# Optimization experiments

Measured on AMD Instinct MI355X. Metric: run time of the kernel, lower is better.

## Reference

```python
import jax, jax.numpy as jnp
import numpy as np

B, T, C = 2, 2048, 1024
NH = 16
HS = C // NH


def setup_inputs() -> dict:
    key = jax.random.key(0)
    k1, k2, k3 = jax.random.split(key, 3)
    scale = 1.0 / np.sqrt(C)
    return {
        "x": jax.random.normal(k1, (B, T, C), dtype=jnp.float32),
        "W_attn": jax.random.normal(k2, (C, 3 * C), dtype=jnp.float32) * scale,
        "b_attn": jnp.zeros((3 * C,), dtype=jnp.float32),
        "W_proj": jax.random.normal(k3, (C, C), dtype=jnp.float32) * scale,
        "b_proj": jnp.zeros((C,), dtype=jnp.float32),
    }


def reference(x, W_attn, b_attn, W_proj, b_proj) -> jnp.ndarray:
    Bx, Tx, Cx = x.shape
    qkv = x @ W_attn + b_attn                      # [B, T, 3C]
    q, k, v = jnp.split(qkv, 3, axis=-1)           # each [B, T, C]

    def heads(t):  # [B, T, C] -> [B, NH, T, HS]
        return t.reshape(Bx, Tx, NH, HS).transpose(0, 2, 1, 3)

    q, k, v = heads(q), heads(k), heads(v)
    att = jnp.einsum("bhqd,bhkd->bhqk", q, k) / jnp.sqrt(jnp.float32(HS))
    causal = jnp.tril(jnp.ones((Tx, Tx), dtype=bool))
    att = jnp.where(causal, att, -jnp.inf)
    att = jax.nn.softmax(att, axis=-1)
    y = jnp.einsum("bhqk,bhkd->bhqd", att, v)      # [B, NH, T, HS]
    y = y.transpose(0, 2, 1, 3).reshape(Bx, Tx, Cx)
    return y @ W_proj + b_proj
```

## Files before the change

kernel.cpp:

```cpp
#include <hip/hip_runtime.h>
#include <hip/hip_bf16.h>
#include <stdint.h>

#define DEV static __device__ __forceinline__

typedef __attribute__((ext_vector_type(8))) __bf16 bf16x8;
typedef __attribute__((ext_vector_type(4))) __bf16 bf16x4;
typedef __attribute__((ext_vector_type(4))) float f32x4;
typedef __attribute__((ext_vector_type(16))) float f32x16;

#define BB 2
#define TT 2048
#define CC 1024
#define NHH 16
#define HSS 64
#define BT 4096
#define N3 3072

DEV unsigned short f2bf(float f) {
  union { float f; uint32_t u; } v; v.f = f;
  uint32_t r = v.u + 0x7FFFu + ((v.u >> 16) & 1u);
  return (unsigned short)(r >> 16);
}

typedef const __attribute__((address_space(1))) unsigned int* gas_t;
typedef __attribute__((address_space(3))) unsigned int* las_t;

DEV void glds16(const void* g, void* l) {
  __builtin_amdgcn_global_load_lds((gas_t)g, (las_t)l, 16, 0, 0);
}

DEV f32x4 mfma16(bf16x8 a, bf16x8 b, f32x4 c) {
  return __builtin_amdgcn_mfma_f32_16x16x32_bf16(a, b, c, 0, 0, 0);
}
DEV f32x16 mfma32(bf16x8 a, bf16x8 b, f32x16 c) {
  return __builtin_amdgcn_mfma_f32_32x32x16_bf16(a, b, c, 0, 0, 0);
}

DEV bf16x8 ld8(const unsigned short* p) { return *(const bf16x8*)p; }

DEV f32x16 z16() {
  f32x16 v;
#pragma unroll
  for (int i = 0; i < 16; i++) v[i] = 0.f;
  return v;
}

__global__ __launch_bounds__(256) void k_prep(const float* __restrict__ x,
                                              const float* __restrict__ Wa,
                                              const float* __restrict__ Wp,
                                              unsigned short* __restrict__ xb,
                                              unsigned short* __restrict__ wabt,
                                              unsigned short* __restrict__ wpbt) {
  const int bid = blockIdx.x;
  const int t = threadIdx.x;
  if (bid < 1024) {
    int i = bid * 256 + t;
    const int n4 = BT * CC / 4;
#pragma unroll
    for (int r = 0; r < 4; r++, i += 262144) {
      if (i < n4) {
        float4 v = ((const float4*)x)[i];
        ushort4 o;
        o.x = f2bf(v.x); o.y = f2bf(v.y); o.z = f2bf(v.z); o.w = f2bf(v.w);
        ((ushort4*)xb)[i] = o;
      }
    }
    return;
  }
  __shared__ float tile[32][33];
  const float* in;
  unsigned short* out;
  int N, tid;
  if (bid < 4096) { in = Wa; out = wabt; N = N3; tid = bid - 1024; }
  else            { in = Wp; out = wpbt; N = CC; tid = bid - 4096; }
  const int ntx = N / 32;
  const int n0 = (tid % ntx) * 32, k0 = (tid / ntx) * 32;
  const int tx = t & 31, ty = t >> 5;
  for (int r = ty; r < 32; r += 8)
    tile[r][tx] = in[(size_t)(k0 + r) * N + n0 + tx];
  __syncthreads();
  for (int r = ty; r < 32; r += 8)
    out[(size_t)(n0 + r) * CC + k0 + tx] = f2bf(tile[tx][r]);
}

template <int OUT_BF16>
__global__ __launch_bounds__(512) void k_gemm(const unsigned short* __restrict__ A,
                                              const unsigned short* __restrict__ Bt,
                                              const float* __restrict__ bias,
                                              void* __restrict__ Cout,
                                              unsigned short* __restrict__ vtOut,
                                              int N, int K, int Rm, int Rn, int Xn) {
  __shared__ __align__(16) unsigned short As[3][128 * 32];
  __shared__ __align__(16) unsigned short Bs[3][128 * 32];
  const int t = threadIdx.x;
  const int wave = t >> 6, l = t & 63, lr = l & 15, lg = l >> 4;
  const int xcd = (int)blockIdx.x & 7, q = (int)blockIdx.x >> 3;
  const int m0 = ((xcd / Xn) * Rm + (q % Rm)) * 128;
  const int n0 = ((xcd % Xn) * Rn + (q / Rm)) * 128;
  const int wm = wave >> 2, wn = wave & 3;

  f32x4 acc[4][2] = {};

  const unsigned short* gA = A + (size_t)(m0 + (t >> 2)) * K + (t & 3) * 8;
  const unsigned short* gB = Bt + (size_t)(n0 + (t >> 2)) * K + (t & 3) * 8;

#define GSTAGE(buf_, k_)                                                  \
  do {                                                                    \
    glds16(gA + (k_), (char*)As[buf_] + t * 16);                          \
    glds16(gB + (k_), (char*)Bs[buf_] + t * 16);                          \
  } while (0)

  const int nst = K >> 5;
  GSTAGE(0, 0);
  GSTAGE(1, 32);

  for (int st = 0; st < nst; ++st) {
    __builtin_amdgcn_s_barrier();
    __builtin_amdgcn_sched_barrier(0);
    if (st + 2 < nst) GSTAGE((st + 2) % 3, (st + 2) * 32);
    __builtin_amdgcn_sched_barrier(0);
    if (st + 2 < nst)      asm volatile("s_waitcnt vmcnt(4)" ::: "memory");
    else if (st + 1 < nst) asm volatile("s_waitcnt vmcnt(2)" ::: "memory");
    else                   asm volatile("s_waitcnt vmcnt(0)" ::: "memory");
    __builtin_amdgcn_s_barrier();
    __builtin_amdgcn_sched_barrier(0);

    const unsigned short* Ab = As[st % 3];
    const unsigned short* Bb = Bs[st % 3];
    bf16x8 av[4], bv[2];
#pragma unroll
    for (int i = 0; i < 4; i++)
      av[i] = ld8(Ab + (wm * 64 + i * 16 + lr) * 32 + lg * 8);
#pragma unroll
    for (int j = 0; j < 2; j++)
      bv[j] = ld8(Bb + (wn * 32 + j * 16 + lr) * 32 + lg * 8);
    __builtin_amdgcn_s_setprio(1);
#pragma unroll
    for (int i = 0; i < 4; i++)
#pragma unroll
      for (int j = 0; j < 2; j++)
        acc[i][j] = mfma16(av[i], bv[j], acc[i][j]);
    __builtin_amdgcn_s_setprio(0);
  }
#undef GSTAGE

  if (OUT_BF16 && vtOut != nullptr && n0 >= 2 * CC) {
#pragma unroll
    for (int j2 = 0; j2 < 2; j2++) {
      int cv = n0 - 2 * CC + wn * 32 + j2 * 16 + lr;
      int h = cv >> 6, d = cv & 63;
      float bv_ = bias[2 * CC + cv];
#pragma unroll
      for (int i = 0; i < 4; i++) {
        int row = m0 + wm * 64 + i * 16 + lg * 4;
        int bb = row >> 11, t2 = row & 2047;
        ushort4 wv;
        wv.x = f2bf(acc[i][j2][0] + bv_);
        wv.y = f2bf(acc[i][j2][1] + bv_);
        wv.z = f2bf(acc[i][j2][2] + bv_);
        wv.w = f2bf(acc[i][j2][3] + bv_);
        *(ushort4*)(vtOut + (((size_t)(bb * NHH + h) * HSS + d) << 11) + t2) = wv;
      }
    }
    return;
  }

#pragma unroll
  for (int j2 = 0; j2 < 2; j2++) {
    int col = n0 + wn * 32 + j2 * 16 + lr;
    float bv_ = bias[col];
#pragma unroll
    for (int i = 0; i < 4; i++) {
      int row = m0 + wm * 64 + i * 16 + lg * 4;
#pragma unroll
      for (int r = 0; r < 4; r++) {
        float v = acc[i][j2][r] + bv_;
        if (OUT_BF16)
          ((unsigned short*)Cout)[(size_t)(row + r) * N + col] = f2bf(v);
        else
          ((float*)Cout)[(size_t)(row + r) * N + col] = v;
      }
    }
  }
}

__global__ __launch_bounds__(512) void k_attn(const unsigned short* __restrict__ qkv,
                                              const unsigned short* __restrict__ vt,
                                              unsigned short* __restrict__ y) {
  __shared__ __align__(16) unsigned short Ks[3][128 * 64];
  __shared__ __align__(16) unsigned short Vs[3][128 * 64];
  __shared__ __align__(16) unsigned short Ps[8][32 * 64];
  __shared__ float Msh[4][64];
  __shared__ float Lsh[4][64];
  const int t = threadIdx.x;
  const int w = t >> 6, l = t & 63, lq = l & 31, hl = l >> 5;
  const int qsub = w & 3, par = w >> 2;
  const int id = blockIdx.x;
  const int bh = (id & 7) + 8 * ((id >> 3) & 3);
  const int p = id >> 5;
  const int b = bh >> 4, head = bh & 15;
  const int jA = 15 - p, jB = p;
  const int mA = jA + 1;
  const int NT = 17;
  const float cexp = 0.18033688011112042f;
  const float THR = 40.0f;

#define SWZ(r_) ((((r_) & 7) ^ (((r_) >> 3) & 3)) << 4)

  const int myswz = SWZ(lq);
  int offs[4];
#pragma unroll
  for (int s = 0; s < 4; s++) offs[s] = (32 * s + 16 * hl) ^ myswz;

  const int off0 = w * 1024 + l * 16;
  const int off1 = 8192 + w * 1024 + l * 16;
  const int rk0 = off0 >> 7, rk1 = off1 >> 7;
  const int ck0 = (off0 & 127) ^ SWZ(rk0), ck1 = (off1 & 127) ^ SWZ(rk1);
  const int rv0 = rk0 & 63, rv1 = rk1 & 63;
  const int cv0 = (off0 & 127) ^ SWZ(rv0), cv1 = (off1 & 127) ^ SWZ(rv1);
  const char* gK0 = (const char*)(qkv + (size_t)(b * TT + rk0) * N3 + CC + head * HSS) + ck0;
  const char* gK1 = (const char*)(qkv + (size_t)(b * TT + rk1) * N3 + CC + head * HSS) + ck1;
  const char* gV0 = (const char*)(vt + ((size_t)bh * HSS + rv0) * TT) + cv0;
  const char* gV1 = (const char*)(vt + ((size_t)bh * HSS + rv1) * TT + 64) + cv1;
  const int dK0 = w * 1024, dK1 = 8192 + w * 1024;

#define STAGE(slot_, kvt_)                                                \
  do {                                                                    \
    size_t kb = (size_t)(kvt_) * (128 * N3 * 2);                          \
    size_t vb = (size_t)(kvt_) * 256;                                     \
    glds16(gK0 + kb, (char*)Ks[slot_] + dK0);                             \
    glds16(gK1 + kb, (char*)Ks[slot_] + dK1);                             \
    glds16(gV0 + vb, (char*)Vs[slot_] + dK0);                             \
    glds16(gV1 + vb, (char*)Vs[slot_] + dK1);                             \
  } while (0)

#define WRITE_OUT()                                                       \
  do {                                                                    \
    float l_q = l_ln + __shfl_xor(l_ln, 32);                              \
    float inv = 1.0f / l_q;                                               \
    unsigned short* ybase = y + (size_t)(b * TT + q0w + lq) * CC + head * HSS; \
    _Pragma("unroll")                                                     \
    for (int g = 0; g < 4; g++) {                                         \
      ushort4 wv;                                                         \
      wv.x = f2bf(oa[4 * g + 0] * inv); wv.y = f2bf(oa[4 * g + 1] * inv); \
      wv.z = f2bf(oa[4 * g + 2] * inv); wv.w = f2bf(oa[4 * g + 3] * inv); \
      *(ushort4*)(ybase + 8 * g + 4 * hl) = wv;                           \
      ushort4 wv2;                                                        \
      wv2.x = f2bf(ob[4 * g + 0] * inv); wv2.y = f2bf(ob[4 * g + 1] * inv); \
      wv2.z = f2bf(ob[4 * g + 2] * inv); wv2.w = f2bf(ob[4 * g + 3] * inv); \
      *(ushort4*)(ybase + 32 + 8 * g + 4 * hl) = wv2;                     \
    }                                                                     \
  } while (0)

#define MERGE()                                                           \
  do {                                                                    \
    __builtin_amdgcn_s_barrier();                                         \
    if (par) {                                                            \
      float* poa = (float*)Ps[w];                                         \
      float* pob = (float*)Ps[w - 4];                                     \
      _Pragma("unroll")                                                   \
      for (int g = 0; g < 16; g++) { poa[g * 64 + l] = oa[g]; pob[g * 64 + l] = ob[g]; } \
      Msh[qsub][l] = m_s; Lsh[qsub][l] = l_ln;                            \
    }                                                                     \
    asm volatile("s_waitcnt lgkmcnt(0)" ::: "memory");                    \
    __builtin_amdgcn_s_barrier();                                         \
    __builtin_amdgcn_sched_barrier(0);                                    \
    if (!par) {                                                           \
      float m1 = Msh[qsub][l], l1 = Lsh[qsub][l];                         \
      float mstar = fmaxf(m_s, m1);                                       \
      float a0 = __builtin_amdgcn_exp2f((m_s - mstar) * cexp);            \
      float a1 = __builtin_amdgcn_exp2f((m1 - mstar) * cexp);             \
      const float* poa = (const float*)Ps[w + 4];                         \
      const float* pob = (const float*)Ps[w];                             \
      _Pragma("unroll")                                                   \
      for (int g = 0; g < 16; g++) {                                      \
        oa[g] = oa[g] * a0 + poa[g * 64 + l] * a1;                        \
        ob[g] = ob[g] * a0 + pob[g * 64 + l] * a1;                        \
      }                                                                   \
      l_ln = l_ln * a0 + l1 * a1;                                         \
      WRITE_OUT();                                                        \
    }                                                                     \
    __builtin_amdgcn_s_barrier();                                         \
  } while (0)

  int q0w = jA * 128 + qsub * 32;
  const unsigned short* qp = qkv + (size_t)(b * TT + q0w + lq) * N3 + head * HSS + hl * 8;
  bf16x8 qf0 = ld8(qp), qf1 = ld8(qp + 16), qf2 = ld8(qp + 32), qf3 = ld8(qp + 48);
  float m_s = -INFINITY, l_ln = 0.f;
  f32x16 oa = z16(), ob = z16();
  char* prow = (char*)Ps[w] + lq * 128;

  STAGE(0, 0);
  int cur = 0;

  for (int seq = 0; seq < NT; ++seq) {
    if (seq == mA) {
      MERGE();
      q0w = jB * 128 + qsub * 32;
      const unsigned short* qp2 = qkv + (size_t)(b * TT + q0w + lq) * N3 + head * HSS + hl * 8;
      qf0 = ld8(qp2); qf1 = ld8(qp2 + 16); qf2 = ld8(qp2 + 32); qf3 = ld8(qp2 + 48);
      m_s = -INFINITY; l_ln = 0.f;
      oa = z16(); ob = z16();
    }

    const int kvt = (seq < mA) ? seq : (seq - mA);
    if (seq + 1 < NT) {
      int s2 = seq + 1;
      int kvt2 = (s2 < mA) ? s2 : (s2 - mA);
      int nxt = (cur == 2) ? 0 : cur + 1;
      STAGE(nxt, kvt2);
      __builtin_amdgcn_sched_barrier(0);
      asm volatile("s_waitcnt vmcnt(4)" ::: "memory");
    } else {
      asm volatile("s_waitcnt vmcnt(0)" ::: "memory");
    }
    __builtin_amdgcn_s_barrier();
    __builtin_amdgcn_sched_barrier(0);

    const int mybuf = cur;
    cur = (cur == 2) ? 0 : cur + 1;

    const int kv0w = kvt * 128 + 64 * par;
    if (kv0w > q0w + 31) continue;

    const unsigned short* Kb = Ks[mybuf];
    const unsigned short* Vb = Vs[mybuf];

    const char* krA = (const char*)Kb + (64 * par + lq) * 128;
    const char* krB = krA + 32 * 128;
    f32x16 sa = z16(), sb = z16();
    __builtin_amdgcn_s_setprio(1);
    {
      bf16x8 ka, kb8;
      ka = ld8((const unsigned short*)(krA + offs[0]));
      kb8 = ld8((const unsigned short*)(krB + offs[0]));
      sa = mfma32(ka, qf0, sa); sb = mfma32(kb8, qf0, sb);
      ka = ld8((const unsigned short*)(krA + offs[1]));
      kb8 = ld8((const unsigned short*)(krB + offs[1]));
      sa = mfma32(ka, qf1, sa); sb = mfma32(kb8, qf1, sb);
      ka = ld8((const unsigned short*)(krA + offs[2]));
      kb8 = ld8((const unsigned short*)(krB + offs[2]));
      sa = mfma32(ka, qf2, sa); sb = mfma32(kb8, qf2, sb);
      ka = ld8((const unsigned short*)(krA + offs[3]));
      kb8 = ld8((const unsigned short*)(krB + offs[3]));
      sa = mfma32(ka, qf3, sa); sb = mfma32(kb8, qf3, sb);
    }
    __builtin_amdgcn_s_setprio(0);

    if (kv0w + 63 > q0w) {
      const int q = q0w + lq;
#pragma unroll
      for (int g = 0; g < 16; g++) {
        int kvl = kv0w + (g & 3) + 8 * (g >> 2) + 4 * hl;
        if (kvl > q) sa[g] = -INFINITY;
        if (kvl + 32 > q) sb[g] = -INFINITY;
      }
    }

    float tmax = -INFINITY;
#pragma unroll
    for (int g = 0; g < 16; g++) tmax = fmaxf(tmax, fmaxf(sa[g], sb[g]));
    tmax = fmaxf(tmax, __shfl_xor(tmax, 32));

    if (!__all(tmax <= m_s + THR)) {
      float m_new = fmaxf(m_s, tmax);
      float alpha = __builtin_amdgcn_exp2f((m_s - m_new) * cexp);
      l_ln *= alpha;
#pragma unroll
      for (int g = 0; g < 16; g++) { oa[g] *= alpha; ob[g] *= alpha; }
      m_s = m_new;
    }

    const float mc = m_s * cexp;
    float tsum = 0.f;
#pragma unroll
    for (int g = 0; g < 16; g++) {
      sa[g] = __builtin_amdgcn_exp2f(__builtin_fmaf(sa[g], cexp, -mc));
      sb[g] = __builtin_amdgcn_exp2f(__builtin_fmaf(sb[g], cexp, -mc));
      tsum += sa[g] + sb[g];
    }
    l_ln += tsum;

#pragma unroll
    for (int u2 = 0; u2 < 4; u2++) {
      bf16x4 w0, w1;
#pragma unroll
      for (int r = 0; r < 4; r++) { w0[r] = (__bf16)sa[4 * u2 + r]; w1[r] = (__bf16)sb[4 * u2 + r]; }
      *(bf16x4*)(prow + ((16 * u2 + 8 * hl) ^ myswz)) = w0;
      *(bf16x4*)(prow + ((64 + 16 * u2 + 8 * hl) ^ myswz)) = w1;
    }
    asm volatile("s_waitcnt lgkmcnt(0)" ::: "memory");
    __builtin_amdgcn_sched_barrier(0);
    bf16x8 pf0 = ld8((const unsigned short*)(prow + offs[0]));
    bf16x8 pf1 = ld8((const unsigned short*)(prow + offs[1]));
    bf16x8 pf2 = ld8((const unsigned short*)(prow + offs[2]));
    bf16x8 pf3 = ld8((const unsigned short*)(prow + offs[3]));

    const char* vrA = (const char*)Vb + par * 8192 + lq * 128;
    const char* vrB = vrA + 32 * 128;
    __builtin_amdgcn_s_setprio(1);
    {
      bf16x8 va, vb8;
      va = ld8((const unsigned short*)(vrA + offs[0]));
      vb8 = ld8((const unsigned short*)(vrB + offs[0]));
      oa = mfma32(va, pf0, oa); ob = mfma32(vb8, pf0, ob);
      va = ld8((const unsigned short*)(vrA + offs[1]));
      vb8 = ld8((const unsigned short*)(vrB + offs[1]));
      oa = mfma32(va, pf1, oa); ob = mfma32(vb8, pf1, ob);
      va = ld8((const unsigned short*)(vrA + offs[2]));
      vb8 = ld8((const unsigned short*)(vrB + offs[2]));
      oa = mfma32(va, pf2, oa); ob = mfma32(vb8, pf2, ob);
      va = ld8((const unsigned short*)(vrA + offs[3]));
      vb8 = ld8((const unsigned short*)(vrB + offs[3]));
      oa = mfma32(va, pf3, oa); ob = mfma32(vb8, pf3, ob);
    }
    __builtin_amdgcn_s_setprio(0);
  }

  MERGE();
#undef STAGE
#undef WRITE_OUT
#undef MERGE
#undef SWZ
}

extern "C" void kernel_launch(void* const* d_in, const int* in_sizes, int n_in,
                              void* d_out, int out_size, void* d_ws, size_t ws_size,
                              hipStream_t stream) {
  const float* x = (const float*)d_in[0];
  const float* W_attn = (const float*)d_in[1];
  const float* b_attn = (const float*)d_in[2];
  const float* W_proj = (const float*)d_in[3];
  const float* b_proj = (const float*)d_in[4];

  char* ws = (char*)d_ws;
  unsigned short* xb   = (unsigned short*)(ws);
  unsigned short* wabt = (unsigned short*)(ws + 8388608);
  unsigned short* wpbt = (unsigned short*)(ws + 14680064);
  unsigned short* qkvb = (unsigned short*)(ws + 16777216);
  unsigned short* vt   = (unsigned short*)(ws + 41943040);
  unsigned short* yb   = (unsigned short*)(ws + 50331648);

  k_prep<<<dim3(5120), 256, 0, stream>>>(x, W_attn, W_proj, xb, wabt, wpbt);
  k_gemm<1><<<dim3(768), 512, 0, stream>>>(xb, wabt, b_attn, qkvb, vt, N3, CC, 8, 12, 2);
  k_attn<<<dim3(256), 512, 0, stream>>>(qkvb, vt, yb);
  k_gemm<0><<<dim3(256), 512, 0, stream>>>(yb, wpbt, b_proj, d_out, nullptr, CC, CC, 4, 8, 1);
}
```

Measured before the change: 106.4 us.

## Load V directly from global memory and double-buffer only K in LDS

Removes the LDS staging of the transposed V tile. Each wave now reads its V fragments straight from global memory (through L1/L2) inside the PV MFMA loop. K staging drops from a triple to a double buffer, with an extra barrier at the top of each iteration so a slot is not overwritten while still in use. This cuts LDS footprint and async copy traffic, which may allow more occupancy. The cost is exposed global-load latency right before the PV MFMAs and one more barrier per tile.

```diff
diff --git a/kernel.cpp b/kernel.cpp
--- a/kernel.cpp
+++ b/kernel.cpp
@@ -188,8 +188,7 @@
 __global__ __launch_bounds__(512) void k_attn(const unsigned short* __restrict__ qkv,
                                               const unsigned short* __restrict__ vt,
                                               unsigned short* __restrict__ y) {
-  __shared__ __align__(16) unsigned short Ks[3][128 * 64];
-  __shared__ __align__(16) unsigned short Vs[3][128 * 64];
+  __shared__ __align__(16) unsigned short Ks[2][128 * 64];
   __shared__ __align__(16) unsigned short Ps[8][32 * 64];
   __shared__ float Msh[4][64];
   __shared__ float Lsh[4][64];
@@ -217,22 +216,18 @@
   const int off1 = 8192 + w * 1024 + l * 16;
   const int rk0 = off0 >> 7, rk1 = off1 >> 7;
   const int ck0 = (off0 & 127) ^ SWZ(rk0), ck1 = (off1 & 127) ^ SWZ(rk1);
-  const int rv0 = rk0 & 63, rv1 = rk1 & 63;
-  const int cv0 = (off0 & 127) ^ SWZ(rv0), cv1 = (off1 & 127) ^ SWZ(rv1);
   const char* gK0 = (const char*)(qkv + (size_t)(b * TT + rk0) * N3 + CC + head * HSS) + ck0;
   const char* gK1 = (const char*)(qkv + (size_t)(b * TT + rk1) * N3 + CC + head * HSS) + ck1;
-  const char* gV0 = (const char*)(vt + ((size_t)bh * HSS + rv0) * TT) + cv0;
-  const char* gV1 = (const char*)(vt + ((size_t)bh * HSS + rv1) * TT + 64) + cv1;
   const int dK0 = w * 1024, dK1 = 8192 + w * 1024;
+
+  const unsigned short* vgA = vt + ((size_t)bh * HSS + lq) * TT;
+  const unsigned short* vgB = vgA + (size_t)32 * TT;
 
 #define STAGE(slot_, kvt_)                                                \
   do {                                                                    \
     size_t kb = (size_t)(kvt_) * (128 * N3 * 2);                          \
-    size_t vb = (size_t)(kvt_) * 256;                                     \
     glds16(gK0 + kb, (char*)Ks[slot_] + dK0);                             \
     glds16(gK1 + kb, (char*)Ks[slot_] + dK1);                             \
-    glds16(gV0 + vb, (char*)Vs[slot_] + dK0);                             \
-    glds16(gV1 + vb, (char*)Vs[slot_] + dK1);                             \
   } while (0)
 
 #define WRITE_OUT()                                                       \
@@ -292,7 +287,6 @@
   char* prow = (char*)Ps[w] + lq * 128;
 
   STAGE(0, 0);
-  int cur = 0;
 
   for (int seq = 0; seq < NT; ++seq) {
     if (seq == mA) {
@@ -304,28 +298,24 @@
       oa = z16(); ob = z16();
     }
 
-    const int kvt = (seq < mA) ? seq : (seq - mA);
+    __builtin_amdgcn_s_barrier();
+    __builtin_amdgcn_sched_barrier(0);
     if (seq + 1 < NT) {
       int s2 = seq + 1;
       int kvt2 = (s2 < mA) ? s2 : (s2 - mA);
-      int nxt = (cur == 2) ? 0 : cur + 1;
-      STAGE(nxt, kvt2);
-      __builtin_amdgcn_sched_barrier(0);
-      asm volatile("s_waitcnt vmcnt(4)" ::: "memory");
-    } else {
-      asm volatile("s_waitcnt vmcnt(0)" ::: "memory");
-    }
+      STAGE(s2 & 1, kvt2);
+    }
+    __builtin_amdgcn_sched_barrier(0);
+    if (seq + 1 < NT) asm volatile("s_waitcnt vmcnt(2)" ::: "memory");
+    else              asm volatile("s_waitcnt vmcnt(0)" ::: "memory");
     __builtin_amdgcn_s_barrier();
     __builtin_amdgcn_sched_barrier(0);
 
-    const int mybuf = cur;
-    cur = (cur == 2) ? 0 : cur + 1;
-
+    const int kvt = (seq < mA) ? seq : (seq - mA);
     const int kv0w = kvt * 128 + 64 * par;
     if (kv0w > q0w + 31) continue;
 
-    const unsigned short* Kb = Ks[mybuf];
-    const unsigned short* Vb = Vs[mybuf];
+    const unsigned short* Kb = Ks[seq & 1];
 
     const char* krA = (const char*)Kb + (64 * par + lq) * 128;
     const char* krB = krA + 32 * 128;
@@ -397,25 +387,22 @@
     bf16x8 pf2 = ld8((const unsigned short*)(prow + offs[2]));
     bf16x8 pf3 = ld8((const unsigned short*)(prow + offs[3]));
 
-    const char* vrA = (const char*)Vb + par * 8192 + lq * 128;
-    const char* vrB = vrA + 32 * 128;
+    const unsigned short* vA = vgA + kv0w + 8 * hl;
+    const unsigned short* vB = vgB + kv0w + 8 * hl;
     __builtin_amdgcn_s_setprio(1);
     {
       bf16x8 va, vb8;
-      va = ld8((const unsigned short*)(vrA + offs[0]));
-      vb8 = ld8((const unsigned short*)(vrB + offs[0]));
+      va = ld8(vA);       vb8 = ld8(vB);
       oa = mfma32(va, pf0, oa); ob = mfma32(vb8, pf0, ob);
-      va = ld8((const unsigned short*)(vrA + offs[1]));
-      vb8 = ld8((const unsigned short*)(vrB + offs[1]));
+      va = ld8(vA + 16);  vb8 = ld8(vB + 16);
       oa = mfma32(va, pf1, oa); ob = mfma32(vb8, pf1, ob);
-      va = ld8((const unsigned short*)(vrA + offs[2]));
-      vb8 = ld8((const unsigned short*)(vrB + offs[2]));
+      va = ld8(vA + 32);  vb8 = ld8(vB + 32);
       oa = mfma32(va, pf2, oa); ob = mfma32(vb8, pf2, ob);
-      va = ld8((const unsigned short*)(vrA + offs[3]));
-      vb8 = ld8((const unsigned short*)(vrB + offs[3]));
+      va = ld8(vA + 48);  vb8 = ld8(vB + 48);
       oa = mfma32(va, pf3, oa); ob = mfma32(vb8, pf3, ob);
     }
     __builtin_amdgcn_s_setprio(0);
+    __builtin_amdgcn_sched_barrier(0);
   }
 
   MERGE();
```

Result: slower. 128.2 us (+20.6%).
